# Optimization experiments

Measured on AMD Instinct MI355X. Metric: run time of the kernel, lower is better.

The kernel has to match this reference:

```python
import jax, jax.numpy as jnp
import numpy as np

B, T, H, L, V = 256, 1024, 256, 128, 13  # V = FDIM_JOINT_VOCAB_DECODING


def setup_inputs() -> dict:
    key = jax.random.key(0)
    ks = jax.random.split(key, 16)
    s = lambda *sh: 1.0 / np.sqrt(sh[-1])
    inp = {
        "seq_input": jax.random.normal(ks[0], (B, T, V), jnp.float32),
        "latent_vec": jax.random.normal(ks[1], (B, L), jnp.float32),
        "labels": jax.random.randint(ks[2], (B, T), 0, V, jnp.int32),
        "lengths": jax.random.randint(ks[3], (B,), 1, T, jnp.int32),
        # latent_vec_linear: L -> H
        "W_lat": jax.random.normal(ks[4], (H, L), jnp.float32) * s(H, L),
        "b_lat": jnp.zeros((H,), jnp.float32),
        # LSTMCell (PyTorch gate order i,f,g,o)
        "W_ih": jax.random.normal(ks[5], (4 * H, V), jnp.float32) * s(4 * H, V),
        "W_hh": jax.random.normal(ks[6], (4 * H, H), jnp.float32) * s(4 * H, H),
        "b_ih": jnp.zeros((4 * H,), jnp.float32),
        "b_hh": jnp.zeros((4 * H,), jnp.float32),
        # W_nonlinear: H+L -> H
        "W_nl": jax.random.normal(ks[7], (H, H + L), jnp.float32) * s(H, H + L),
        "b_nl": jnp.zeros((H,), jnp.float32),
        # W: H -> V
        "W_out": jax.random.normal(ks[8], (V, H), jnp.float32) * s(V, H),
        "b_out": jnp.zeros((V,), jnp.float32),
    }
    return inp


def _forward(seq_input, latent_vec, labels, lengths,
             W_lat, b_lat, W_ih, W_hh, b_ih, b_hh, W_nl, b_nl, W_out, b_out):
    h0 = jax.nn.relu(latent_vec @ W_lat.T + b_lat)          # [B,H]
    c0 = jnp.zeros_like(h0)

    def step(carry, x_t):
        h, c = carry
        gates = x_t @ W_ih.T + b_ih + h @ W_hh.T + b_hh     # [B,4H]
        i, f, g, o = jnp.split(gates, 4, axis=-1)
        c = jax.nn.sigmoid(f) * c + jax.nn.sigmoid(i) * jnp.tanh(g)
        h = jax.nn.sigmoid(o) * jnp.tanh(c)
        return (h, c), h

    xs = jnp.swapaxes(seq_input, 0, 1)                      # [T,B,V]
    _, hs = jax.lax.scan(step, (h0, c0), xs)                # [T,B,H]
    hs = jnp.swapaxes(hs, 0, 1)                             # [B,T,H]

    lat = jnp.broadcast_to(latent_vec[:, None, :], (B, T, L))
    feats = jnp.concatenate([hs, lat], axis=-1)             # [B,T,H+L]
    logits = jax.nn.relu(feats @ W_nl.T + b_nl) @ W_out.T + b_out  # [B,T,V]

    logp = jax.nn.log_softmax(logits, axis=-1)
    nll = -jnp.take_along_axis(logp, labels[..., None], axis=-1)[..., 0]  # [B,T]
    mask = (jnp.arange(T)[None, :] < lengths[:, None]).astype(nll.dtype)
    batch_loss = jnp.sum(nll * mask, axis=1)                # [B]
    return batch_loss


def reference(seq_input, latent_vec, labels, lengths,
              W_lat, b_lat, W_ih, W_hh, b_ih, b_hh, W_nl, b_nl, W_out, b_out):
    return _forward(seq_input, latent_vec, labels, lengths,
                    W_lat, b_lat, W_ih, W_hh, b_ih, b_hh, W_nl, b_nl, W_out, b_out)
```

## Files before the change

kernel.cpp:

```cpp
#include <hip/hip_runtime.h>
#include <hip/hip_fp16.h>

#define NB 256
#define NT 1024
#define NH 256
#define NL 128
#define NV 13

typedef _Float16 h2t __attribute__((ext_vector_type(2)));
typedef _Float16 f16x8 __attribute__((ext_vector_type(8)));
typedef float f32x4 __attribute__((ext_vector_type(4)));

#define WS_WHH   0x0u
#define WS_WIH   0x80000u
#define WS_BIAS  0x88000u
#define WS_H0F   0x89000u
#define WS_LATF  0xA9000u
#define WS_WNL   0xB9000u
#define WS_WOUT  0xE9000u
#define WS_HS    0x100000u

__device__ __forceinline__ unsigned pk2(float a, float b){
  union { h2t h; unsigned u; } u;
  u.h.x = (_Float16)a; u.h.y = (_Float16)b;
  return u.u;
}

__device__ __forceinline__ float fdot2u(unsigned a, unsigned b, float c){
  union { unsigned u; h2t h; } ua, ub;
  ua.u = a; ub.u = b;
  return __builtin_amdgcn_fdot2(ua.h, ub.h, c, false);
}

__device__ __forceinline__ float sigm(float x){ return __builtin_amdgcn_rcpf(1.f + __expf(-x)); }
__device__ __forceinline__ float tanh_(float x){ return 2.f*__builtin_amdgcn_rcpf(1.f + __expf(-2.f*x)) - 1.f; }

__global__ void k_prep(const float* __restrict__ Wih, const float* __restrict__ Whh,
                       const float* __restrict__ bih, const float* __restrict__ bhh,
                       const float* __restrict__ Wnl, const float* __restrict__ Wout,
                       unsigned char* __restrict__ ws){
  unsigned* whh = (unsigned*)(ws + WS_WHH);
  unsigned* wih = (unsigned*)(ws + WS_WIH);
  float* bias   = (float*)(ws + WS_BIAS);
  unsigned* wnl = (unsigned*)(ws + WS_WNL);
  unsigned* wout= (unsigned*)(ws + WS_WOUT);
  int blk = blockIdx.x, tid = threadIdx.x;
  if (blk < 1024){
    int r = blk;
    if (tid < 128) whh[r*128+tid] = pk2(Whh[r*256+2*tid], Whh[r*256+2*tid+1]);
    if (tid < 8){
      int k0 = 2*tid, k1 = 2*tid+1;
      float a = (k0 < NV)? Wih[r*NV+k0] : 0.f;
      float b = (k1 < NV)? Wih[r*NV+k1] : 0.f;
      wih[r*8+tid] = pk2(a,b);
    }
    if (tid == 0) bias[r] = bih[r] + bhh[r];
  } else if (blk < 1280){
    int n = blk - 1024;
    for (int i = tid; i < 192; i += 128)
      wnl[n*192+i] = pk2(Wnl[n*384+2*i], Wnl[n*384+2*i+1]);
  } else {
    for (int i = tid; i < 2048; i += 128){
      int v = i >> 7; int p = (i & 127)*2;
      float a = (v < NV)? Wout[v*256+p]   : 0.f;
      float b = (v < NV)? Wout[v*256+p+1] : 0.f;
      wout[i] = pk2(a,b);
    }
  }
}

__global__ void k_init(const float* __restrict__ lat, const float* __restrict__ Wlat,
                       const float* __restrict__ blat, unsigned char* __restrict__ ws,
                       float* __restrict__ out){
  __shared__ float sl[NL];
  int b = blockIdx.x, j = threadIdx.x;
  if (j < NL) sl[j] = lat[b*NL+j];
  __syncthreads();
  float a = blat[j];
  for (int k = 0; k < NL; ++k) a += Wlat[j*NL+k]*sl[k];
  float h0 = a > 0.f ? a : 0.f;
  __half* h0h    = (__half*)(ws + WS_H0F);
  unsigned* latf = (unsigned*)(ws + WS_LATF);
  h0h[b*256+j] = __float2half(h0);
  if (j < 64)  latf[b*64+j] = pk2(sl[2*j], sl[2*j+1]);
  if (j == 0)  out[b] = 0.f;
}

__global__ __launch_bounds__(512) __attribute__((amdgpu_waves_per_eu(2, 2)))
void k_lstm(const float* __restrict__ seq, unsigned char* __restrict__ ws){
  __shared__ __align__(16) uint4 lws[9][2][512];
  __shared__ __align__(16) __half h2s[256];
  __shared__ __align__(8)  float gts2[256][2];
  __shared__ __align__(16) unsigned xb[2][8];
  int b = blockIdx.x, j = threadIdx.x;
  int lane = j & 63;
  int r0 = j, r1 = j + 512;
  const uint4* whh4 = (const uint4*)(ws + WS_WHH);
  const uint4* wih4 = (const uint4*)(ws + WS_WIH);
  const float* bias = (const float*)(ws + WS_BIAS);
  const __half* h0h = (const __half*)(ws + WS_H0F);
  __half* hs = (__half*)(ws + WS_HS);

  uint4 wv[2][7];
  unsigned ag[2][16][4];
  uint4 wx[2][2];
  float bb0, bb1;
#pragma unroll
  for (int rr = 0; rr < 2; ++rr){
    int r = (rr == 0)? r0 : r1;
#pragma unroll
    for (int q = 0; q < 7; ++q) wv[rr][q] = whh4[r*32+q];
#pragma unroll
    for (int q = 0; q < 16; ++q){
      uint4 w = whh4[r*32+7+q];
      asm volatile("v_accvgpr_write_b32 %0, %1" : "=a"(ag[rr][q][0]) : "v"(w.x));
      asm volatile("v_accvgpr_write_b32 %0, %1" : "=a"(ag[rr][q][1]) : "v"(w.y));
      asm volatile("v_accvgpr_write_b32 %0, %1" : "=a"(ag[rr][q][2]) : "v"(w.z));
      asm volatile("v_accvgpr_write_b32 %0, %1" : "=a"(ag[rr][q][3]) : "v"(w.w));
    }
#pragma unroll
    for (int q = 0; q < 9; ++q) lws[q][rr][j] = whh4[r*32+23+q];
    wx[rr][0] = wih4[r*2]; wx[rr][1] = wih4[r*2+1];
  }
  bb0 = bias[r0]; bb1 = bias[r1];
  if (j < 256){
    h2s[j] = h0h[b*256+j];
  }
  if (j >= 256 && j < 264){
    int i2 = j - 256; int k0 = 2*i2;
    const float* xp = seq + (size_t)b*NT*NV;
    float xa = (k0   < NV)? xp[k0]   : 0.f;
    float xc = (k0+1 < NV)? xp[k0+1] : 0.f;
    xb[0][i2] = pk2(xa, xc);
  }
  float c = 0.f;
#pragma unroll
  for (int rr = 0; rr < 2; ++rr){
#pragma unroll
    for (int q = 0; q < 7; ++q)
      asm volatile("" : "+v"(wv[rr][q].x), "+v"(wv[rr][q].y), "+v"(wv[rr][q].z), "+v"(wv[rr][q].w));
    asm volatile("" : "+v"(wx[rr][0].x), "+v"(wx[rr][0].y), "+v"(wx[rr][0].z), "+v"(wx[rr][0].w));
    asm volatile("" : "+v"(wx[rr][1].x), "+v"(wx[rr][1].y), "+v"(wx[rr][1].z), "+v"(wx[rr][1].w));
  }
  __syncthreads();
  const unsigned* h32 = (const unsigned*)h2s;

#pragma unroll 1
  for (int t = 0; t < NT; ++t){
    float xna = 0.f, xnc = 0.f;
    bool doX = (j >= 256 && j < 264) && (t+1 < NT);
    if (doX){
      int k0 = 2*(j-256);
      const float* xp = seq + ((size_t)b*NT + (t+1))*NV;
      xna = (k0   < NV)? xp[k0]   : 0.f;
      xnc = (k0+1 < NV)? xp[k0+1] : 0.f;
    }
    unsigned vh0 = h32[lane];
    unsigned vh1 = h32[lane + 64];
    float p00 = bb0, p01 = 0.f;
    float p10 = bb1, p11 = 0.f;
    {
      const uint4* xc4 = (const uint4*)xb[t & 1];
      uint4 x0 = xc4[0], x1 = xc4[1];
      p00 = fdot2u(wx[0][0].x, x0.x, p00); p01 = fdot2u(wx[0][0].y, x0.y, p01);
      p00 = fdot2u(wx[0][0].z, x0.z, p00); p01 = fdot2u(wx[0][0].w, x0.w, p01);
      p00 = fdot2u(wx[0][1].x, x1.x, p00); p01 = fdot2u(wx[0][1].y, x1.y, p01);
      p00 = fdot2u(wx[0][1].z, x1.z, p00);
      p10 = fdot2u(wx[1][0].x, x0.x, p10); p11 = fdot2u(wx[1][0].y, x0.y, p11);
      p10 = fdot2u(wx[1][0].z, x0.z, p10); p11 = fdot2u(wx[1][0].w, x0.w, p11);
      p10 = fdot2u(wx[1][1].x, x1.x, p10); p11 = fdot2u(wx[1][1].y, x1.y, p11);
      p10 = fdot2u(wx[1][1].z, x1.z, p10);
    }
#pragma unroll
    for (int q = 0; q < 7; ++q){
      unsigned h0 = __builtin_amdgcn_readlane(vh0, 4*q+0);
      unsigned h1 = __builtin_amdgcn_readlane(vh0, 4*q+1);
      unsigned h2 = __builtin_amdgcn_readlane(vh0, 4*q+2);
      unsigned h3 = __builtin_amdgcn_readlane(vh0, 4*q+3);
      p00 = fdot2u(wv[0][q].x, h0, p00); p01 = fdot2u(wv[0][q].y, h1, p01);
      p00 = fdot2u(wv[0][q].z, h2, p00); p01 = fdot2u(wv[0][q].w, h3, p01);
      p10 = fdot2u(wv[1][q].x, h0, p10); p11 = fdot2u(wv[1][q].y, h1, p11);
      p10 = fdot2u(wv[1][q].z, h2, p10); p11 = fdot2u(wv[1][q].w, h3, p11);
    }
#pragma unroll
    for (int q = 0; q < 16; ++q){
      const int base = 28 + 4*q;
      unsigned h0 = __builtin_amdgcn_readlane((base+0) < 64 ? vh0 : vh1, (base+0) & 63);
      unsigned h1 = __builtin_amdgcn_readlane((base+1) < 64 ? vh0 : vh1, (base+1) & 63);
      unsigned h2 = __builtin_amdgcn_readlane((base+2) < 64 ? vh0 : vh1, (base+2) & 63);
      unsigned h3 = __builtin_amdgcn_readlane((base+3) < 64 ? vh0 : vh1, (base+3) & 63);
      unsigned t0, t1, t2, t3, t4, t5, t6, t7;
      asm volatile("v_accvgpr_read_b32 %0, %1" : "=v"(t0) : "a"(ag[0][q][0]));
      asm volatile("v_accvgpr_read_b32 %0, %1" : "=v"(t1) : "a"(ag[0][q][1]));
      asm volatile("v_accvgpr_read_b32 %0, %1" : "=v"(t2) : "a"(ag[0][q][2]));
      asm volatile("v_accvgpr_read_b32 %0, %1" : "=v"(t3) : "a"(ag[0][q][3]));
      asm volatile("v_accvgpr_read_b32 %0, %1" : "=v"(t4) : "a"(ag[1][q][0]));
      asm volatile("v_accvgpr_read_b32 %0, %1" : "=v"(t5) : "a"(ag[1][q][1]));
      asm volatile("v_accvgpr_read_b32 %0, %1" : "=v"(t6) : "a"(ag[1][q][2]));
      asm volatile("v_accvgpr_read_b32 %0, %1" : "=v"(t7) : "a"(ag[1][q][3]));
      p00 = fdot2u(t0, h0, p00); p01 = fdot2u(t1, h1, p01);
      p00 = fdot2u(t2, h2, p00); p01 = fdot2u(t3, h3, p01);
      p10 = fdot2u(t4, h0, p10); p11 = fdot2u(t5, h1, p11);
      p10 = fdot2u(t6, h2, p10); p11 = fdot2u(t7, h3, p11);
    }
#pragma unroll
    for (int q = 0; q < 9; ++q){
      const int base = 92 + 4*q;
      unsigned h0 = __builtin_amdgcn_readlane(vh1, (base+0) - 64);
      unsigned h1 = __builtin_amdgcn_readlane(vh1, (base+1) - 64);
      unsigned h2 = __builtin_amdgcn_readlane(vh1, (base+2) - 64);
      unsigned h3 = __builtin_amdgcn_readlane(vh1, (base+3) - 64);
      uint4 wa = lws[q][0][j];
      uint4 wb = lws[q][1][j];
      p00 = fdot2u(wa.x, h0, p00); p01 = fdot2u(wa.y, h1, p01);
      p00 = fdot2u(wa.z, h2, p00); p01 = fdot2u(wa.w, h3, p01);
      p10 = fdot2u(wb.x, h0, p10); p11 = fdot2u(wb.y, h1, p11);
      p10 = fdot2u(wb.z, h2, p10); p11 = fdot2u(wb.w, h3, p11);
    }
    float a0 = p00 + p01;
    float a1 = p10 + p11;
    if (j >= 256){ *(float2*)gts2[j-256] = make_float2(a0, a1); }
    __syncthreads();
    if (j < 256){
      float2 fo = *(const float2*)gts2[j];
      c = sigm(fo.x)*c + sigm(a0)*tanh_(a1);
      float h = sigm(fo.y)*tanh_(c);
      __half hh = __float2half(h);
      h2s[j] = hh;
      hs[((size_t)b*NT + t)*NH + j] = hh;
    }
    if (doX) xb[(t+1) & 1][j-256] = pk2(xna, xnc);
    __syncthreads();
  }
}

struct __align__(16) SMp {
  union {
    struct { __half As[128][72]; __half Bs[256][72]; } s;
    __half Zs[128][264];
  } u;
  unsigned wout[16][128];
  float bnl[256];
  float bout[16];
  float logit[128][16];
  float red[128];
};

__global__ __launch_bounds__(512, 2)
void k_proj(const unsigned char* __restrict__ ws,
            const int* __restrict__ labels, const int* __restrict__ lengths,
            const float* __restrict__ bnl, const float* __restrict__ bout,
            float* __restrict__ out){
  __shared__ SMp sm;
  int tid = threadIdx.x;
  int mt = blockIdx.x;
  int m0 = mt*128;
  int b  = m0 >> 10;
  int t0 = m0 & 1023;
  const __half* hs      = (const __half*)(ws + WS_HS);
  const unsigned* latf  = (const unsigned*)(ws + WS_LATF);
  const unsigned* wnl   = (const unsigned*)(ws + WS_WNL);
  const unsigned* woutg = (const unsigned*)(ws + WS_WOUT);

  for (int i = tid; i < 2048; i += 512) ((unsigned*)sm.wout)[i] = woutg[i];
  if (tid < 256) sm.bnl[tid] = bnl[tid];
  if (tid < 16)  sm.bout[tid] = (tid < NV)? bout[tid] : 0.f;

  int wave = tid >> 6, lane = tid & 63;
  int wm = wave >> 2, wn = wave & 3;
  int l15 = lane & 15, l4 = lane >> 4;

  f32x4 acc[4][4];
  f32x4 zz = {0.f,0.f,0.f,0.f};
#pragma unroll
  for (int a = 0; a < 4; ++a)
#pragma unroll
    for (int q = 0; q < 4; ++q) acc[a][q] = zz;

#pragma unroll 1
  for (int kt = 0; kt < 6; ++kt){
#pragma unroll
    for (int it = 0; it < 2; ++it){
      int idx = it*512 + tid;
      int r = idx >> 3, ck = idx & 7;
      int k = kt*64 + ck*8;
      uint4 val;
      if (k < 256) val = *(const uint4*)&hs[((size_t)(m0+r))*NH + k];
      else         val = *(const uint4*)&latf[b*64 + (k-256)/2];
      *(uint4*)&sm.u.s.As[r][ck*8] = val;
    }
#pragma unroll
    for (int it = 0; it < 4; ++it){
      int idx = it*512 + tid;
      int n = idx >> 3, ck = idx & 7;
      int k = kt*64 + ck*8;
      uint4 val = *(const uint4*)&wnl[n*192 + k/2];
      *(uint4*)&sm.u.s.Bs[n][ck*8] = val;
    }
    __syncthreads();
#pragma unroll
    for (int kk = 0; kk < 2; ++kk){
      f16x8 af[4], bf[4];
#pragma unroll
      for (int mf = 0; mf < 4; ++mf) af[mf] = *(const f16x8*)&sm.u.s.As[wm*64+mf*16+l15][kk*32+l4*8];
#pragma unroll
      for (int nf = 0; nf < 4; ++nf) bf[nf] = *(const f16x8*)&sm.u.s.Bs[wn*64+nf*16+l15][kk*32+l4*8];
#pragma unroll
      for (int mf = 0; mf < 4; ++mf)
#pragma unroll
        for (int nf = 0; nf < 4; ++nf)
          acc[mf][nf] = __builtin_amdgcn_mfma_f32_16x16x32_f16(af[mf], bf[nf], acc[mf][nf], 0, 0, 0);
    }
    __syncthreads();
  }

#pragma unroll
  for (int mf = 0; mf < 4; ++mf)
#pragma unroll
    for (int nf = 0; nf < 4; ++nf)
#pragma unroll
      for (int e = 0; e < 4; ++e){
        int row = wm*64 + mf*16 + l4*4 + e;
        int col = wn*64 + nf*16 + l15;
        float v = acc[mf][nf][e] + sm.bnl[col];
        v = v > 0.f ? v : 0.f;
        sm.u.Zs[row][col] = __float2half(v);
      }
  __syncthreads();

  int r = tid >> 2, q = tid & 3;
  float la0 = sm.bout[q], la1 = sm.bout[q+4], la2 = sm.bout[q+8], la3 = sm.bout[q+12];
#pragma unroll
  for (int c8 = 0; c8 < 32; ++c8){
    uint4 zv = *(const uint4*)&sm.u.Zs[r][c8*8];
    uint4 w0 = *(const uint4*)&sm.wout[q][c8*4];
    uint4 w1 = *(const uint4*)&sm.wout[q+4][c8*4];
    uint4 w2 = *(const uint4*)&sm.wout[q+8][c8*4];
    uint4 w3 = *(const uint4*)&sm.wout[q+12][c8*4];
    la0 = fdot2u(w0.x, zv.x, la0); la0 = fdot2u(w0.y, zv.y, la0);
    la0 = fdot2u(w0.z, zv.z, la0); la0 = fdot2u(w0.w, zv.w, la0);
    la1 = fdot2u(w1.x, zv.x, la1); la1 = fdot2u(w1.y, zv.y, la1);
    la1 = fdot2u(w1.z, zv.z, la1); la1 = fdot2u(w1.w, zv.w, la1);
    la2 = fdot2u(w2.x, zv.x, la2); la2 = fdot2u(w2.y, zv.y, la2);
    la2 = fdot2u(w2.z, zv.z, la2); la2 = fdot2u(w2.w, zv.w, la2);
    la3 = fdot2u(w3.x, zv.x, la3); la3 = fdot2u(w3.y, zv.y, la3);
    la3 = fdot2u(w3.z, zv.z, la3); la3 = fdot2u(w3.w, zv.w, la3);
  }
  sm.logit[r][q] = la0; sm.logit[r][q+4] = la1; sm.logit[r][q+8] = la2; sm.logit[r][q+12] = la3;
  __syncthreads();

  if (tid < 128){
    int t = t0 + tid;
    float mx = -1e30f;
#pragma unroll
    for (int v = 0; v < NV; ++v) mx = fmaxf(mx, sm.logit[tid][v]);
    float s = 0.f;
#pragma unroll
    for (int v = 0; v < NV; ++v) s += __expf(sm.logit[tid][v] - mx);
    float lse = mx + __logf(s);
    int lab = labels[b*NT + t];
    float nll = lse - sm.logit[tid][lab];
    sm.red[tid] = (t < lengths[b])? nll : 0.f;
  }
  __syncthreads();
  if (tid < 64){
    float v = sm.red[tid] + sm.red[tid+64];
#pragma unroll
    for (int off = 32; off > 0; off >>= 1) v += __shfl_down(v, off);
    if (tid == 0) atomicAdd(out + b, v);
  }
}

extern "C" void kernel_launch(void* const* d_in, const int* in_sizes, int n_in,
                              void* d_out, int out_size, void* d_ws, size_t ws_size,
                              hipStream_t stream){
  const float* seq   = (const float*)d_in[0];
  const float* lat   = (const float*)d_in[1];
  const int* labels  = (const int*)d_in[2];
  const int* lengths = (const int*)d_in[3];
  const float* Wlat  = (const float*)d_in[4];
  const float* blat  = (const float*)d_in[5];
  const float* Wih   = (const float*)d_in[6];
  const float* Whh   = (const float*)d_in[7];
  const float* bih   = (const float*)d_in[8];
  const float* bhh   = (const float*)d_in[9];
  const float* Wnl   = (const float*)d_in[10];
  const float* bnl   = (const float*)d_in[11];
  const float* Wout  = (const float*)d_in[12];
  const float* bout  = (const float*)d_in[13];
  float* out = (float*)d_out;
  unsigned char* ws = (unsigned char*)d_ws;

  hipLaunchKernelGGL(k_prep, dim3(1281), dim3(128), 0, stream, Wih, Whh, bih, bhh, Wnl, Wout, ws);
  hipLaunchKernelGGL(k_init, dim3(256), dim3(256), 0, stream, lat, Wlat, blat, ws, out);
  hipLaunchKernelGGL(k_lstm, dim3(256), dim3(512), 0, stream, seq, ws);
  hipLaunchKernelGGL(k_proj, dim3(2048), dim3(512), 0, stream, ws, labels, lengths, bnl, bout, out);
}
```

Baseline: 2.591 ms.

## Pair gate rows across adjacent lanes and exchange via DPP, dropping one barrier

Gate rows are reassigned so each lane pair holds all four gates (i,g and f,o) of one hidden unit, and partial gate values are swapped with a DPP quad permute instead of going through shared memory. This removes one of the two __syncthreads per timestep. The h buffer is double-buffered to keep reads and writes race-free with the single barrier. Part of the h broadcast now uses uint4 LDS reads instead of readlane. Both lanes of a pair now compute the activations redundantly, and only even lanes write h.

```diff
diff --git a/kernel.cpp b/kernel.cpp
--- a/kernel.cpp
+++ b/kernel.cpp
@@ -34,6 +34,12 @@
 
 __device__ __forceinline__ float sigm(float x){ return __builtin_amdgcn_rcpf(1.f + __expf(-x)); }
 __device__ __forceinline__ float tanh_(float x){ return 2.f*__builtin_amdgcn_rcpf(1.f + __expf(-2.f*x)) - 1.f; }
+
+__device__ __forceinline__ float dpp_swap1(float x){
+  int xi = __builtin_bit_cast(int, x);
+  int y = __builtin_amdgcn_mov_dpp(xi, 0xB1, 0xF, 0xF, true);
+  return __builtin_bit_cast(float, y);
+}
 
 __global__ void k_prep(const float* __restrict__ Wih, const float* __restrict__ Whh,
                        const float* __restrict__ bih, const float* __restrict__ bhh,
@@ -89,12 +95,13 @@
 __global__ __launch_bounds__(512) __attribute__((amdgpu_waves_per_eu(2, 2)))
 void k_lstm(const float* __restrict__ seq, unsigned char* __restrict__ ws){
   __shared__ __align__(16) uint4 lws[9][2][512];
-  __shared__ __align__(16) __half h2s[256];
-  __shared__ __align__(8)  float gts2[256][2];
+  __shared__ __align__(16) __half h2s[2][256];
   __shared__ __align__(16) unsigned xb[2][8];
   int b = blockIdx.x, j = threadIdx.x;
   int lane = j & 63;
-  int r0 = j, r1 = j + 512;
+  int u = j >> 1, p = j & 1;
+  int row0 = u + 256*p;
+  int row1 = row0 + 512;
   const uint4* whh4 = (const uint4*)(ws + WS_WHH);
   const uint4* wih4 = (const uint4*)(ws + WS_WIH);
   const float* bias = (const float*)(ws + WS_BIAS);
@@ -107,7 +114,7 @@
   float bb0, bb1;
 #pragma unroll
   for (int rr = 0; rr < 2; ++rr){
-    int r = (rr == 0)? r0 : r1;
+    int r = (rr == 0)? row0 : row1;
 #pragma unroll
     for (int q = 0; q < 7; ++q) wv[rr][q] = whh4[r*32+q];
 #pragma unroll
@@ -122,10 +129,8 @@
     for (int q = 0; q < 9; ++q) lws[q][rr][j] = whh4[r*32+23+q];
     wx[rr][0] = wih4[r*2]; wx[rr][1] = wih4[r*2+1];
   }
-  bb0 = bias[r0]; bb1 = bias[r1];
-  if (j < 256){
-    h2s[j] = h0h[b*256+j];
-  }
+  bb0 = bias[row0]; bb1 = bias[row1];
+  if (j < 256) h2s[0][j] = h0h[b*256+j];
   if (j >= 256 && j < 264){
     int i2 = j - 256; int k0 = 2*i2;
     const float* xp = seq + (size_t)b*NT*NV;
@@ -143,10 +148,11 @@
     asm volatile("" : "+v"(wx[rr][1].x), "+v"(wx[rr][1].y), "+v"(wx[rr][1].z), "+v"(wx[rr][1].w));
   }
   __syncthreads();
-  const unsigned* h32 = (const unsigned*)h2s;
 
 #pragma unroll 1
   for (int t = 0; t < NT; ++t){
+    const unsigned* h32 = (const unsigned*)h2s[t & 1];
+    const uint4*    h4  = (const uint4*)h2s[t & 1];
     float xna = 0.f, xnc = 0.f;
     bool doX = (j >= 256 && j < 264) && (t+1 < NT);
     if (doX){
@@ -183,51 +189,67 @@
       p10 = fdot2u(wv[1][q].z, h2, p10); p11 = fdot2u(wv[1][q].w, h3, p11);
     }
 #pragma unroll
-    for (int q = 0; q < 16; ++q){
-      const int base = 28 + 4*q;
+    for (int q = 7; q < 20; ++q){
+      const int base = 4*q;
       unsigned h0 = __builtin_amdgcn_readlane((base+0) < 64 ? vh0 : vh1, (base+0) & 63);
       unsigned h1 = __builtin_amdgcn_readlane((base+1) < 64 ? vh0 : vh1, (base+1) & 63);
       unsigned h2 = __builtin_amdgcn_readlane((base+2) < 64 ? vh0 : vh1, (base+2) & 63);
       unsigned h3 = __builtin_amdgcn_readlane((base+3) < 64 ? vh0 : vh1, (base+3) & 63);
       unsigned t0, t1, t2, t3, t4, t5, t6, t7;
-      asm volatile("v_accvgpr_read_b32 %0, %1" : "=v"(t0) : "a"(ag[0][q][0]));
-      asm volatile("v_accvgpr_read_b32 %0, %1" : "=v"(t1) : "a"(ag[0][q][1]));
-      asm volatile("v_accvgpr_read_b32 %0, %1" : "=v"(t2) : "a"(ag[0][q][2]));
-      asm volatile("v_accvgpr_read_b32 %0, %1" : "=v"(t3) : "a"(ag[0][q][3]));
-      asm volatile("v_accvgpr_read_b32 %0, %1" : "=v"(t4) : "a"(ag[1][q][0]));
-      asm volatile("v_accvgpr_read_b32 %0, %1" : "=v"(t5) : "a"(ag[1][q][1]));
-      asm volatile("v_accvgpr_read_b32 %0, %1" : "=v"(t6) : "a"(ag[1][q][2]));
-      asm volatile("v_accvgpr_read_b32 %0, %1" : "=v"(t7) : "a"(ag[1][q][3]));
+      asm volatile("v_accvgpr_read_b32 %0, %1" : "=v"(t0) : "a"(ag[0][q-7][0]));
+      asm volatile("v_accvgpr_read_b32 %0, %1" : "=v"(t1) : "a"(ag[0][q-7][1]));
+      asm volatile("v_accvgpr_read_b32 %0, %1" : "=v"(t2) : "a"(ag[0][q-7][2]));
+      asm volatile("v_accvgpr_read_b32 %0, %1" : "=v"(t3) : "a"(ag[0][q-7][3]));
+      asm volatile("v_accvgpr_read_b32 %0, %1" : "=v"(t4) : "a"(ag[1][q-7][0]));
+      asm volatile("v_accvgpr_read_b32 %0, %1" : "=v"(t5) : "a"(ag[1][q-7][1]));
+      asm volatile("v_accvgpr_read_b32 %0, %1" : "=v"(t6) : "a"(ag[1][q-7][2]));
+      asm volatile("v_accvgpr_read_b32 %0, %1" : "=v"(t7) : "a"(ag[1][q-7][3]));
       p00 = fdot2u(t0, h0, p00); p01 = fdot2u(t1, h1, p01);
       p00 = fdot2u(t2, h2, p00); p01 = fdot2u(t3, h3, p01);
       p10 = fdot2u(t4, h0, p10); p11 = fdot2u(t5, h1, p11);
       p10 = fdot2u(t6, h2, p10); p11 = fdot2u(t7, h3, p11);
     }
 #pragma unroll
+    for (int q = 20; q < 23; ++q){
+      uint4 hq = h4[q];
+      unsigned t0, t1, t2, t3, t4, t5, t6, t7;
+      asm volatile("v_accvgpr_read_b32 %0, %1" : "=v"(t0) : "a"(ag[0][q-7][0]));
+      asm volatile("v_accvgpr_read_b32 %0, %1" : "=v"(t1) : "a"(ag[0][q-7][1]));
+      asm volatile("v_accvgpr_read_b32 %0, %1" : "=v"(t2) : "a"(ag[0][q-7][2]));
+      asm volatile("v_accvgpr_read_b32 %0, %1" : "=v"(t3) : "a"(ag[0][q-7][3]));
+      asm volatile("v_accvgpr_read_b32 %0, %1" : "=v"(t4) : "a"(ag[1][q-7][0]));
+      asm volatile("v_accvgpr_read_b32 %0, %1" : "=v"(t5) : "a"(ag[1][q-7][1]));
+      asm volatile("v_accvgpr_read_b32 %0, %1" : "=v"(t6) : "a"(ag[1][q-7][2]));
+      asm volatile("v_accvgpr_read_b32 %0, %1" : "=v"(t7) : "a"(ag[1][q-7][3]));
+      p00 = fdot2u(t0, hq.x, p00); p01 = fdot2u(t1, hq.y, p01);
+      p00 = fdot2u(t2, hq.z, p00); p01 = fdot2u(t3, hq.w, p01);
+      p10 = fdot2u(t4, hq.x, p10); p11 = fdot2u(t5, hq.y, p11);
+      p10 = fdot2u(t6, hq.z, p10); p11 = fdot2u(t7, hq.w, p11);
+    }
+#pragma unroll
     for (int q = 0; q < 9; ++q){
-      const int base = 92 + 4*q;
-      unsigned h0 = __builtin_amdgcn_readlane(vh1, (base+0) - 64);
-      unsigned h1 = __builtin_amdgcn_readlane(vh1, (base+1) - 64);
-      unsigned h2 = __builtin_amdgcn_readlane(vh1, (base+2) - 64);
-      unsigned h3 = __builtin_amdgcn_readlane(vh1, (base+3) - 64);
+      uint4 hq = h4[23+q];
       uint4 wa = lws[q][0][j];
       uint4 wb = lws[q][1][j];
-      p00 = fdot2u(wa.x, h0, p00); p01 = fdot2u(wa.y, h1, p01);
-      p00 = fdot2u(wa.z, h2, p00); p01 = fdot2u(wa.w, h3, p01);
-      p10 = fdot2u(wb.x, h0, p10); p11 = fdot2u(wb.y, h1, p11);
-      p10 = fdot2u(wb.z, h2, p10); p11 = fdot2u(wb.w, h3, p11);
+      p00 = fdot2u(wa.x, hq.x, p00); p01 = fdot2u(wa.y, hq.y, p01);
+      p00 = fdot2u(wa.z, hq.z, p00); p01 = fdot2u(wa.w, hq.w, p01);
+      p10 = fdot2u(wb.x, hq.x, p10); p11 = fdot2u(wb.y, hq.y, p11);
+      p10 = fdot2u(wb.z, hq.z, p10); p11 = fdot2u(wb.w, hq.w, p11);
     }
     float a0 = p00 + p01;
     float a1 = p10 + p11;
-    if (j >= 256){ *(float2*)gts2[j-256] = make_float2(a0, a1); }
-    __syncthreads();
-    if (j < 256){
-      float2 fo = *(const float2*)gts2[j];
-      c = sigm(fo.x)*c + sigm(a0)*tanh_(a1);
-      float h = sigm(fo.y)*tanh_(c);
+    float b0 = dpp_swap1(a0);
+    float b1 = dpp_swap1(a1);
+    float gi = p ? b0 : a0;
+    float gf = p ? a0 : b0;
+    float gg = p ? b1 : a1;
+    float go = p ? a1 : b1;
+    c = sigm(gf)*c + sigm(gi)*tanh_(gg);
+    float h = sigm(go)*tanh_(c);
+    if (p == 0){
       __half hh = __float2half(h);
-      h2s[j] = hh;
-      hs[((size_t)b*NT + t)*NH + j] = hh;
+      h2s[(t+1) & 1][u] = hh;
+      hs[((size_t)b*NT + t)*NH + u] = hh;
     }
     if (doX) xb[(t+1) & 1][j-256] = pk2(xna, xnc);
     __syncthreads();
```

After: 2.805 ms. 8.3% more time.
